# Kernel optimization log

Measured on AMD Instinct MI355X. Metric: run time of the kernel, lower is better.

## Reference

```python
import jax, jax.numpy as jnp
import numpy as np

B = 2048          # batch
F = 32            # input feature size
H = 512           # lstm hidden size
BN = 64           # autoencoder bottleneck
OUT = 8           # final dense output size
SEQ_LEN = 128
LOOK_AHEAD = 32
RS, RE = 0, 8     # replace_start, replace_end (RE-RS == OUT)


def setup_inputs() -> dict:
    key = jax.random.key(0)
    ks = jax.random.split(key, 16)
    s = lambda k, shape: (jax.random.normal(k, shape, jnp.float32) * 0.05)
    return {
        'x': jax.random.normal(ks[0], (B, SEQ_LEN + LOOK_AHEAD, F), jnp.float32),
        # layer-0 LSTMCell (input F)
        'Wih0': s(ks[1], (F, 4 * H)), 'Whh0': s(ks[2], (H, 4 * H)),
        'bih0': s(ks[3], (4 * H,)),   'bhh0': s(ks[4], (4 * H,)),
        # layer-1 LSTMCell (input H)
        'Wih1': s(ks[5], (H, 4 * H)), 'Whh1': s(ks[6], (H, 4 * H)),
        'bih1': s(ks[7], (4 * H,)),   'bhh1': s(ks[8], (4 * H,)),
        # discretizing autoencoder: 2H -> BN -> 2H (shared across layers)
        'We': s(ks[9], (2 * H, BN)),  'be': s(ks[10], (BN,)),
        'Wd': s(ks[11], (BN, 2 * H)), 'bd': s(ks[12], (2 * H,)),
        # final dense H -> OUT
        'Wf': s(ks[13], (H, OUT)),    'bf': s(ks[14], (OUT,)),
    }


def _lstm_cell(x, h, c, Wih, Whh, bih, bhh):
    # torch.nn.LSTMCell gate order: i, f, g, o
    g = x @ Wih + bih + h @ Whh + bhh          # [B, 4H]
    i, f, gg, o = jnp.split(g, 4, axis=1)
    i, f, o = jax.nn.sigmoid(i), jax.nn.sigmoid(f), jax.nn.sigmoid(o)
    c2 = f * c + i * jnp.tanh(gg)
    return o * jnp.tanh(c2), c2


def _ae(z, We, be, Wd, bd):
    # bottleneck with straight-through rounding (discretization)
    b = jnp.tanh(z @ We + be)
    q = b + jax.lax.stop_gradient(jnp.round(b) - b)
    return q @ Wd + bd


def _layers_fwd(x_t, st, p):
    h0, c0, h1, c1 = st
    hc = _ae(jnp.concatenate([h0, c0], axis=1), p['We'], p['be'], p['Wd'], p['bd'])
    h0, c0 = jnp.split(hc, 2, axis=1)
    h0, c0 = _lstm_cell(x_t, h0, c0, p['Wih0'], p['Whh0'], p['bih0'], p['bhh0'])
    # dropout layer between stacked layers is identity in eval mode
    hc = _ae(jnp.concatenate([h1, c1], axis=1), p['We'], p['be'], p['Wd'], p['bd'])
    h1, c1 = jnp.split(hc, 2, axis=1)
    h1, c1 = _lstm_cell(h0, h1, c1, p['Wih1'], p['Whh1'], p['bih1'], p['bhh1'])
    return (h0, c0, h1, c1)


def reference(x, Wih0, Whh0, bih0, bhh0, Wih1, Whh1, bih1, bhh1,
              We, be, Wd, bd, Wf, bf):
    p = dict(Wih0=Wih0, Whh0=Whh0, bih0=bih0, bhh0=bhh0,
             Wih1=Wih1, Whh1=Whh1, bih1=bih1, bhh1=bhh1,
             We=We, be=be, Wd=Wd, bd=bd)
    bsz = x.shape[0]
    z = jnp.zeros((bsz, H), x.dtype)
    st = (z, z, z, z)

    # warm-up phase over seq_len observed steps
    def step1(st, x_t):
        return _layers_fwd(x_t, st, p), None
    st, _ = jax.lax.scan(step1, st, jnp.swapaxes(x[:, :SEQ_LEN], 0, 1))
    out0 = st[2] @ Wf + bf  # final dense on top-layer h

    def step2(carry, x_t):
        st, out = carry
        x_t = x_t.at[:, RS:RE].set(out)
        st = _layers_fwd(x_t, st, p)
        out = st[2] @ Wf + bf
        return (st, out), out
    (_, _), outs = jax.lax.scan(step2, (st, out0),
                                jnp.swapaxes(x[:, SEQ_LEN:SEQ_LEN + LOOK_AHEAD], 0, 1))

    # [B, 1 + look_ahead, OUT]
    return jnp.concatenate([out0[:, None, :], jnp.swapaxes(outs, 0, 1)], axis=1)
```

## Files before the change

### kernel.cpp

```cpp
#include <hip/hip_runtime.h>
#include <hip/hip_bf16.h>
#include <math.h>

#define NB    2048
#define FIN   32
#define HH    512
#define G4    2048
#define BNE   64
#define OUTD  8
#define SEQL  128
#define LOOK  32
#define TOT   (SEQL + LOOK)
#define TB    8
#define NTHR  512

__device__ __forceinline__ float sigf(float v) { return 1.0f / (1.0f + expf(-v)); }

#define MAC8(ACC, W)                                   \
  {                                                    \
    ACC[0] = fmaf(hs0, (W), ACC[0]);                   \
    ACC[1] = fmaf(hs1, (W), ACC[1]);                   \
    ACC[2] = fmaf(hs2, (W), ACC[2]);                   \
    ACC[3] = fmaf(hs3, (W), ACC[3]);                   \
    ACC[4] = fmaf(hs4, (W), ACC[4]);                   \
    ACC[5] = fmaf(hs5, (W), ACC[5]);                   \
    ACC[6] = fmaf(hs6, (W), ACC[6]);                   \
    ACC[7] = fmaf(hs7, (W), ACC[7]);                   \
  }

__global__ __launch_bounds__(NTHR)
void fused_rnn(const float* __restrict__ x,
               const float* __restrict__ Wih0, const float* __restrict__ Whh0,
               const float* __restrict__ bih0, const float* __restrict__ bhh0,
               const float* __restrict__ Wih1, const float* __restrict__ Whh1,
               const float* __restrict__ bih1, const float* __restrict__ bhh1,
               const float* __restrict__ We,   const float* __restrict__ be,
               const float* __restrict__ Wd,   const float* __restrict__ bd,
               const float* __restrict__ Wf,   const float* __restrict__ bf,
               float* __restrict__ out)
{
  __shared__ float sh0[HH][TB], sc0[HH][TB], sh1[HH][TB], sc1[HH][TB];
  __shared__ float sq[2][TB][BNE];
  __shared__ float sx[FIN][TB];
  __shared__ float sout[TB][OUTD];

  const int t  = threadIdx.x;
  const int b0 = blockIdx.x * TB;

  for (int i = t; i < HH * TB; i += NTHR) {
    (&sh0[0][0])[i] = 0.f; (&sc0[0][0])[i] = 0.f;
    (&sh1[0][0])[i] = 0.f; (&sc1[0][0])[i] = 0.f;
  }

  float bias0[4], bias1[4];
#pragma unroll
  for (int j = 0; j < 4; j++) {
    bias0[j] = bih0[j * HH + t] + bhh0[j * HH + t];
    bias1[j] = bih1[j * HH + t] + bhh1[j * HH + t];
  }

  const double Athr = 0.5493061443340549;

  for (int step = 0; step < TOT; ++step) {
    __syncthreads();

    {
      const int ae = t >> 8, s = (t >> 5) & 7, n = t & 31;
      const float* Sh = ae ? &sh1[0][0] : &sh0[0][0];
      const float* Sc = ae ? &sc1[0][0] : &sc0[0][0];
      double a0 = (double)be[n], a1 = (double)be[n + 32];
      const float* we0 = We + n;
#pragma unroll 4
      for (int k = 0; k < HH; k++) {
        double z = (double)Sh[k * TB + s];
        a0 = fma(z, (double)we0[k * BNE], a0);
        a1 = fma(z, (double)we0[k * BNE + 32], a1);
      }
      const float* we1 = We + (size_t)HH * BNE + n;
#pragma unroll 4
      for (int k = 0; k < HH; k++) {
        double z = (double)Sc[k * TB + s];
        a0 = fma(z, (double)we1[k * BNE], a0);
        a1 = fma(z, (double)we1[k * BNE + 32], a1);
      }
      sq[ae][s][n]      = (a0 > Athr) ? 1.f : ((a0 < -Athr) ? -1.f : 0.f);
      sq[ae][s][n + 32] = (a1 > Athr) ? 1.f : ((a1 < -Athr) ? -1.f : 0.f);
    }
    __syncthreads();

    {
      float ah0[TB], ac0[TB], ah1[TB], ac1[TB];
      const float bdh = bd[t], bdc = bd[HH + t];
#pragma unroll
      for (int s = 0; s < TB; s++) { ah0[s] = bdh; ac0[s] = bdc; ah1[s] = bdh; ac1[s] = bdc; }
      const float* wd0 = Wd + t;
      const float* wd1 = Wd + HH + t;
#pragma unroll 2
      for (int j = 0; j < BNE; j++) {
        const float w0 = wd0[j * (2 * HH)];
        const float w1 = wd1[j * (2 * HH)];
#pragma unroll
        for (int s = 0; s < TB; s++) {
          float q0 = sq[0][s][j], q1 = sq[1][s][j];
          ah0[s] = fmaf(q0, w0, ah0[s]); ac0[s] = fmaf(q0, w1, ac0[s]);
          ah1[s] = fmaf(q1, w0, ah1[s]); ac1[s] = fmaf(q1, w1, ac1[s]);
        }
      }
#pragma unroll
      for (int s = 0; s < TB; s++) {
        sh0[t][s] = ah0[s]; sc0[t][s] = ac0[s];
        sh1[t][s] = ah1[s]; sc1[t][s] = ac1[s];
      }
      if (t < FIN * TB) {
        int s = t >> 5, f = t & 31;
        float xv;
        if (step >= SEQL && f < OUTD) xv = sout[s][f];
        else xv = x[((size_t)(b0 + s) * TOT + step) * FIN + f];
        sx[f][s] = xv;
      }
    }
    __syncthreads();

    {
      float accI[TB], accF[TB], accG[TB], accO[TB];
#pragma unroll
      for (int s = 0; s < TB; s++) { accI[s] = bias0[0]; accF[s] = bias0[1]; accG[s] = bias0[2]; accO[s] = bias0[3]; }

      {
        const float* p0 = Wih0 + t;
        const float* p1 = Wih0 + t + 2 * HH;
#pragma unroll 4
        for (int k = 0; k < FIN; k++) {
          float w0 = p0[k * G4], w1 = p0[k * G4 + HH];
          float w2 = p1[k * G4], w3 = p1[k * G4 + HH];
          const float4 hA = *(const float4*)&sx[k][0];
          const float4 hB = *(const float4*)&sx[k][4];
          float hs0 = hA.x, hs1 = hA.y, hs2 = hA.z, hs3 = hA.w;
          float hs4 = hB.x, hs5 = hB.y, hs6 = hB.z, hs7 = hB.w;
          MAC8(accI, w0); MAC8(accF, w1); MAC8(accG, w2); MAC8(accO, w3);
        }
      }
      {
        const float* p0 = Whh0 + t;
        const float* p1 = Whh0 + t + 2 * HH;
#pragma unroll 4
        for (int k = 0; k < HH; k++) {
          float w0 = p0[k * G4], w1 = p0[k * G4 + HH];
          float w2 = p1[k * G4], w3 = p1[k * G4 + HH];
          const float4 hA = *(const float4*)&sh0[k][0];
          const float4 hB = *(const float4*)&sh0[k][4];
          float hs0 = hA.x, hs1 = hA.y, hs2 = hA.z, hs3 = hA.w;
          float hs4 = hB.x, hs5 = hB.y, hs6 = hB.z, hs7 = hB.w;
          MAC8(accI, w0); MAC8(accF, w1); MAC8(accG, w2); MAC8(accO, w3);
        }
      }
      float hn[TB], cn[TB];
      const float4 cA = *(const float4*)&sc0[t][0];
      const float4 cB = *(const float4*)&sc0[t][4];
      float cold[TB] = { cA.x, cA.y, cA.z, cA.w, cB.x, cB.y, cB.z, cB.w };
#pragma unroll
      for (int s = 0; s < TB; s++) {
        float ig = sigf(accI[s]), fg = sigf(accF[s]);
        float gg = tanhf(accG[s]), og = sigf(accO[s]);
        float c2 = fmaf(fg, cold[s], ig * gg);
        cn[s] = c2;
        hn[s] = og * tanhf(c2);
      }
      __syncthreads();
      *(float4*)&sh0[t][0] = make_float4(hn[0], hn[1], hn[2], hn[3]);
      *(float4*)&sh0[t][4] = make_float4(hn[4], hn[5], hn[6], hn[7]);
      *(float4*)&sc0[t][0] = make_float4(cn[0], cn[1], cn[2], cn[3]);
      *(float4*)&sc0[t][4] = make_float4(cn[4], cn[5], cn[6], cn[7]);
    }
    __syncthreads();

    {
      float accI[TB], accF[TB], accG[TB], accO[TB];
#pragma unroll
      for (int s = 0; s < TB; s++) { accI[s] = bias1[0]; accF[s] = bias1[1]; accG[s] = bias1[2]; accO[s] = bias1[3]; }

      {
        const float* p0 = Wih1 + t;
        const float* p1 = Wih1 + t + 2 * HH;
#pragma unroll 4
        for (int k = 0; k < HH; k++) {
          float w0 = p0[k * G4], w1 = p0[k * G4 + HH];
          float w2 = p1[k * G4], w3 = p1[k * G4 + HH];
          const float4 hA = *(const float4*)&sh0[k][0];
          const float4 hB = *(const float4*)&sh0[k][4];
          float hs0 = hA.x, hs1 = hA.y, hs2 = hA.z, hs3 = hA.w;
          float hs4 = hB.x, hs5 = hB.y, hs6 = hB.z, hs7 = hB.w;
          MAC8(accI, w0); MAC8(accF, w1); MAC8(accG, w2); MAC8(accO, w3);
        }
      }
      {
        const float* p0 = Whh1 + t;
        const float* p1 = Whh1 + t + 2 * HH;
#pragma unroll 4
        for (int k = 0; k < HH; k++) {
          float w0 = p0[k * G4], w1 = p0[k * G4 + HH];
          float w2 = p1[k * G4], w3 = p1[k * G4 + HH];
          const float4 hA = *(const float4*)&sh1[k][0];
          const float4 hB = *(const float4*)&sh1[k][4];
          float hs0 = hA.x, hs1 = hA.y, hs2 = hA.z, hs3 = hA.w;
          float hs4 = hB.x, hs5 = hB.y, hs6 = hB.z, hs7 = hB.w;
          MAC8(accI, w0); MAC8(accF, w1); MAC8(accG, w2); MAC8(accO, w3);
        }
      }
      float hn[TB], cn[TB];
      const float4 cA = *(const float4*)&sc1[t][0];
      const float4 cB = *(const float4*)&sc1[t][4];
      float cold[TB] = { cA.x, cA.y, cA.z, cA.w, cB.x, cB.y, cB.z, cB.w };
#pragma unroll
      for (int s = 0; s < TB; s++) {
        float ig = sigf(accI[s]), fg = sigf(accF[s]);
        float gg = tanhf(accG[s]), og = sigf(accO[s]);
        float c2 = fmaf(fg, cold[s], ig * gg);
        cn[s] = c2;
        hn[s] = og * tanhf(c2);
      }
      __syncthreads();
      *(float4*)&sh1[t][0] = make_float4(hn[0], hn[1], hn[2], hn[3]);
      *(float4*)&sh1[t][4] = make_float4(hn[4], hn[5], hn[6], hn[7]);
      *(float4*)&sc1[t][0] = make_float4(cn[0], cn[1], cn[2], cn[3]);
      *(float4*)&sc1[t][4] = make_float4(cn[4], cn[5], cn[6], cn[7]);
    }

    if (step >= SEQL - 1) {
      __syncthreads();
      if (t < TB * OUTD) {
        int s = t >> 3, o = t & 7;
        float a = bf[o];
#pragma unroll 4
        for (int k = 0; k < HH; k++) a = fmaf(sh1[k][s], Wf[k * OUTD + o], a);
        sout[s][o] = a;
        int slot = step - (SEQL - 1);
        out[((size_t)(b0 + s) * (1 + LOOK) + slot) * OUTD + o] = a;
      }
    }
  }
}

extern "C" void kernel_launch(void* const* d_in, const int* in_sizes, int n_in,
                              void* d_out, int out_size, void* d_ws, size_t ws_size,
                              hipStream_t stream) {
  const float* x    = (const float*)d_in[0];
  const float* Wih0 = (const float*)d_in[1];
  const float* Whh0 = (const float*)d_in[2];
  const float* bih0 = (const float*)d_in[3];
  const float* bhh0 = (const float*)d_in[4];
  const float* Wih1 = (const float*)d_in[5];
  const float* Whh1 = (const float*)d_in[6];
  const float* bih1 = (const float*)d_in[7];
  const float* bhh1 = (const float*)d_in[8];
  const float* We   = (const float*)d_in[9];
  const float* be   = (const float*)d_in[10];
  const float* Wd   = (const float*)d_in[11];
  const float* bd   = (const float*)d_in[12];
  const float* Wf   = (const float*)d_in[13];
  const float* bf   = (const float*)d_in[14];

  fused_rnn<<<NB / TB, NTHR, 0, stream>>>(x, Wih0, Whh0, bih0, bhh0,
                                          Wih1, Whh1, bih1, bhh1,
                                          We, be, Wd, bd, Wf, bf,
                                          (float*)d_out);
}
```

Baseline: 89.02 ms.

## Double threads per block and split gate computation via shared gate buffer

Raises the block to 1024 threads. Each thread now computes two adjacent gate columns (float2 weight loads) for all 8 batch rows, writes the pre-activations to a shared gate buffer, and a separate pass applies the LSTM nonlinearities. The encoder and decoder stages are also re-split so each thread handles one bottleneck or output element, and the sq layout is transposed. This exposes more parallelism per recurrent step and gives coalesced float2 weight reads, at the cost of 64KB of extra shared memory, an extra barrier per layer, and fewer registers per thread.

```diff
diff --git a/kernel.cpp b/kernel.cpp
--- a/kernel.cpp
+++ b/kernel.cpp
@@ -12,20 +12,19 @@
 #define LOOK  32
 #define TOT   (SEQL + LOOK)
 #define TB    8
-#define NTHR  512
+#define NTHR  1024
 
 __device__ __forceinline__ float sigf(float v) { return 1.0f / (1.0f + expf(-v)); }
 
-#define MAC8(ACC, W)                                   \
+#define MAC2(S, HS)                                    \
   {                                                    \
-    ACC[0] = fmaf(hs0, (W), ACC[0]);                   \
-    ACC[1] = fmaf(hs1, (W), ACC[1]);                   \
-    ACC[2] = fmaf(hs2, (W), ACC[2]);                   \
-    ACC[3] = fmaf(hs3, (W), ACC[3]);                   \
-    ACC[4] = fmaf(hs4, (W), ACC[4]);                   \
-    ACC[5] = fmaf(hs5, (W), ACC[5]);                   \
-    ACC[6] = fmaf(hs6, (W), ACC[6]);                   \
-    ACC[7] = fmaf(hs7, (W), ACC[7]);                   \
+    a[S].x = fmaf(w.x, (HS), a[S].x);                  \
+    a[S].y = fmaf(w.y, (HS), a[S].y);                  \
+  }
+#define MAC2x8()                                       \
+  {                                                    \
+    MAC2(0, hA.x); MAC2(1, hA.y); MAC2(2, hA.z); MAC2(3, hA.w); \
+    MAC2(4, hB.x); MAC2(5, hB.y); MAC2(6, hB.z); MAC2(7, hB.w); \
   }
 
 __global__ __launch_bounds__(NTHR)
@@ -40,7 +39,8 @@
                float* __restrict__ out)
 {
   __shared__ float sh0[HH][TB], sc0[HH][TB], sh1[HH][TB], sc1[HH][TB];
-  __shared__ float sq[2][TB][BNE];
+  __shared__ float sg[TB][G4];
+  __shared__ float sq[2][BNE][TB];
   __shared__ float sx[FIN][TB];
   __shared__ float sout[TB][OUTD];
 
@@ -52,12 +52,10 @@
     (&sh1[0][0])[i] = 0.f; (&sc1[0][0])[i] = 0.f;
   }
 
-  float bias0[4], bias1[4];
-#pragma unroll
-  for (int j = 0; j < 4; j++) {
-    bias0[j] = bih0[j * HH + t] + bhh0[j * HH + t];
-    bias1[j] = bih1[j * HH + t] + bhh1[j * HH + t];
-  }
+  const float2 bb0 = make_float2(bih0[2*t]   + bhh0[2*t],
+                                 bih0[2*t+1] + bhh0[2*t+1]);
+  const float2 bb1 = make_float2(bih1[2*t]   + bhh1[2*t],
+                                 bih1[2*t+1] + bhh1[2*t+1]);
 
   const double Athr = 0.5493061443340549;
 
@@ -65,51 +63,51 @@
     __syncthreads();
 
     {
-      const int ae = t >> 8, s = (t >> 5) & 7, n = t & 31;
+      const int ae = t >> 9, s = (t >> 6) & 7, n = t & 63;
       const float* Sh = ae ? &sh1[0][0] : &sh0[0][0];
       const float* Sc = ae ? &sc1[0][0] : &sc0[0][0];
-      double a0 = (double)be[n], a1 = (double)be[n + 32];
+      double a0 = (double)be[n];
       const float* we0 = We + n;
 #pragma unroll 4
-      for (int k = 0; k < HH; k++) {
-        double z = (double)Sh[k * TB + s];
-        a0 = fma(z, (double)we0[k * BNE], a0);
-        a1 = fma(z, (double)we0[k * BNE + 32], a1);
-      }
+      for (int k = 0; k < HH; k++)
+        a0 = fma((double)Sh[k * TB + s], (double)we0[(size_t)k * BNE], a0);
       const float* we1 = We + (size_t)HH * BNE + n;
 #pragma unroll 4
-      for (int k = 0; k < HH; k++) {
-        double z = (double)Sc[k * TB + s];
-        a0 = fma(z, (double)we1[k * BNE], a0);
-        a1 = fma(z, (double)we1[k * BNE + 32], a1);
-      }
-      sq[ae][s][n]      = (a0 > Athr) ? 1.f : ((a0 < -Athr) ? -1.f : 0.f);
-      sq[ae][s][n + 32] = (a1 > Athr) ? 1.f : ((a1 < -Athr) ? -1.f : 0.f);
-    }
-    __syncthreads();
-
-    {
-      float ah0[TB], ac0[TB], ah1[TB], ac1[TB];
-      const float bdh = bd[t], bdc = bd[HH + t];
-#pragma unroll
-      for (int s = 0; s < TB; s++) { ah0[s] = bdh; ac0[s] = bdc; ah1[s] = bdh; ac1[s] = bdc; }
-      const float* wd0 = Wd + t;
-      const float* wd1 = Wd + HH + t;
+      for (int k = 0; k < HH; k++)
+        a0 = fma((double)Sc[k * TB + s], (double)we1[(size_t)k * BNE], a0);
+      sq[ae][n][s] = (a0 > Athr) ? 1.f : ((a0 < -Athr) ? -1.f : 0.f);
+    }
+    __syncthreads();
+
+    {
+      float aq0[TB], aq1[TB];
+      const float bdv = bd[t];
+#pragma unroll
+      for (int s = 0; s < TB; s++) { aq0[s] = bdv; aq1[s] = bdv; }
+      const float* wd = Wd + t;
 #pragma unroll 2
       for (int j = 0; j < BNE; j++) {
-        const float w0 = wd0[j * (2 * HH)];
-        const float w1 = wd1[j * (2 * HH)];
-#pragma unroll
-        for (int s = 0; s < TB; s++) {
-          float q0 = sq[0][s][j], q1 = sq[1][s][j];
-          ah0[s] = fmaf(q0, w0, ah0[s]); ac0[s] = fmaf(q0, w1, ac0[s]);
-          ah1[s] = fmaf(q1, w0, ah1[s]); ac1[s] = fmaf(q1, w1, ac1[s]);
-        }
-      }
-#pragma unroll
-      for (int s = 0; s < TB; s++) {
-        sh0[t][s] = ah0[s]; sc0[t][s] = ac0[s];
-        sh1[t][s] = ah1[s]; sc1[t][s] = ac1[s];
+        const float w = wd[(size_t)j * (2 * HH)];
+        const float4 qA0 = *(const float4*)&sq[0][j][0];
+        const float4 qB0 = *(const float4*)&sq[0][j][4];
+        const float4 qA1 = *(const float4*)&sq[1][j][0];
+        const float4 qB1 = *(const float4*)&sq[1][j][4];
+        aq0[0] = fmaf(qA0.x, w, aq0[0]); aq0[1] = fmaf(qA0.y, w, aq0[1]);
+        aq0[2] = fmaf(qA0.z, w, aq0[2]); aq0[3] = fmaf(qA0.w, w, aq0[3]);
+        aq0[4] = fmaf(qB0.x, w, aq0[4]); aq0[5] = fmaf(qB0.y, w, aq0[5]);
+        aq0[6] = fmaf(qB0.z, w, aq0[6]); aq0[7] = fmaf(qB0.w, w, aq0[7]);
+        aq1[0] = fmaf(qA1.x, w, aq1[0]); aq1[1] = fmaf(qA1.y, w, aq1[1]);
+        aq1[2] = fmaf(qA1.z, w, aq1[2]); aq1[3] = fmaf(qA1.w, w, aq1[3]);
+        aq1[4] = fmaf(qB1.x, w, aq1[4]); aq1[5] = fmaf(qB1.y, w, aq1[5]);
+        aq1[6] = fmaf(qB1.z, w, aq1[6]); aq1[7] = fmaf(qB1.w, w, aq1[7]);
+      }
+      if (t < HH) {
+#pragma unroll
+        for (int s = 0; s < TB; s++) { sh0[t][s] = aq0[s]; sh1[t][s] = aq1[s]; }
+      } else {
+        const int c = t - HH;
+#pragma unroll
+        for (int s = 0; s < TB; s++) { sc0[c][s] = aq0[s]; sc1[c][s] = aq1[s]; }
       }
       if (t < FIN * TB) {
         int s = t >> 5, f = t & 31;
@@ -122,108 +120,84 @@
     __syncthreads();
 
     {
-      float accI[TB], accF[TB], accG[TB], accO[TB];
-#pragma unroll
-      for (int s = 0; s < TB; s++) { accI[s] = bias0[0]; accF[s] = bias0[1]; accG[s] = bias0[2]; accO[s] = bias0[3]; }
-
-      {
-        const float* p0 = Wih0 + t;
-        const float* p1 = Wih0 + t + 2 * HH;
-#pragma unroll 4
-        for (int k = 0; k < FIN; k++) {
-          float w0 = p0[k * G4], w1 = p0[k * G4 + HH];
-          float w2 = p1[k * G4], w3 = p1[k * G4 + HH];
-          const float4 hA = *(const float4*)&sx[k][0];
-          const float4 hB = *(const float4*)&sx[k][4];
-          float hs0 = hA.x, hs1 = hA.y, hs2 = hA.z, hs3 = hA.w;
-          float hs4 = hB.x, hs5 = hB.y, hs6 = hB.z, hs7 = hB.w;
-          MAC8(accI, w0); MAC8(accF, w1); MAC8(accG, w2); MAC8(accO, w3);
-        }
-      }
-      {
-        const float* p0 = Whh0 + t;
-        const float* p1 = Whh0 + t + 2 * HH;
-#pragma unroll 4
-        for (int k = 0; k < HH; k++) {
-          float w0 = p0[k * G4], w1 = p0[k * G4 + HH];
-          float w2 = p1[k * G4], w3 = p1[k * G4 + HH];
-          const float4 hA = *(const float4*)&sh0[k][0];
-          const float4 hB = *(const float4*)&sh0[k][4];
-          float hs0 = hA.x, hs1 = hA.y, hs2 = hA.z, hs3 = hA.w;
-          float hs4 = hB.x, hs5 = hB.y, hs6 = hB.z, hs7 = hB.w;
-          MAC8(accI, w0); MAC8(accF, w1); MAC8(accG, w2); MAC8(accO, w3);
-        }
-      }
-      float hn[TB], cn[TB];
-      const float4 cA = *(const float4*)&sc0[t][0];
-      const float4 cB = *(const float4*)&sc0[t][4];
-      float cold[TB] = { cA.x, cA.y, cA.z, cA.w, cB.x, cB.y, cB.z, cB.w };
-#pragma unroll
-      for (int s = 0; s < TB; s++) {
-        float ig = sigf(accI[s]), fg = sigf(accF[s]);
-        float gg = tanhf(accG[s]), og = sigf(accO[s]);
-        float c2 = fmaf(fg, cold[s], ig * gg);
-        cn[s] = c2;
-        hn[s] = og * tanhf(c2);
-      }
-      __syncthreads();
-      *(float4*)&sh0[t][0] = make_float4(hn[0], hn[1], hn[2], hn[3]);
-      *(float4*)&sh0[t][4] = make_float4(hn[4], hn[5], hn[6], hn[7]);
-      *(float4*)&sc0[t][0] = make_float4(cn[0], cn[1], cn[2], cn[3]);
-      *(float4*)&sc0[t][4] = make_float4(cn[4], cn[5], cn[6], cn[7]);
-    }
-    __syncthreads();
-
-    {
-      float accI[TB], accF[TB], accG[TB], accO[TB];
-#pragma unroll
-      for (int s = 0; s < TB; s++) { accI[s] = bias1[0]; accF[s] = bias1[1]; accG[s] = bias1[2]; accO[s] = bias1[3]; }
-
-      {
-        const float* p0 = Wih1 + t;
-        const float* p1 = Wih1 + t + 2 * HH;
-#pragma unroll 4
-        for (int k = 0; k < HH; k++) {
-          float w0 = p0[k * G4], w1 = p0[k * G4 + HH];
-          float w2 = p1[k * G4], w3 = p1[k * G4 + HH];
-          const float4 hA = *(const float4*)&sh0[k][0];
-          const float4 hB = *(const float4*)&sh0[k][4];
-          float hs0 = hA.x, hs1 = hA.y, hs2 = hA.z, hs3 = hA.w;
-          float hs4 = hB.x, hs5 = hB.y, hs6 = hB.z, hs7 = hB.w;
-          MAC8(accI, w0); MAC8(accF, w1); MAC8(accG, w2); MAC8(accO, w3);
-        }
-      }
-      {
-        const float* p0 = Whh1 + t;
-        const float* p1 = Whh1 + t + 2 * HH;
-#pragma unroll 4
-        for (int k = 0; k < HH; k++) {
-          float w0 = p0[k * G4], w1 = p0[k * G4 + HH];
-          float w2 = p1[k * G4], w3 = p1[k * G4 + HH];
-          const float4 hA = *(const float4*)&sh1[k][0];
-          const float4 hB = *(const float4*)&sh1[k][4];
-          float hs0 = hA.x, hs1 = hA.y, hs2 = hA.z, hs3 = hA.w;
-          float hs4 = hB.x, hs5 = hB.y, hs6 = hB.z, hs7 = hB.w;
-          MAC8(accI, w0); MAC8(accF, w1); MAC8(accG, w2); MAC8(accO, w3);
-        }
-      }
-      float hn[TB], cn[TB];
-      const float4 cA = *(const float4*)&sc1[t][0];
-      const float4 cB = *(const float4*)&sc1[t][4];
-      float cold[TB] = { cA.x, cA.y, cA.z, cA.w, cB.x, cB.y, cB.z, cB.w };
-#pragma unroll
-      for (int s = 0; s < TB; s++) {
-        float ig = sigf(accI[s]), fg = sigf(accF[s]);
-        float gg = tanhf(accG[s]), og = sigf(accO[s]);
-        float c2 = fmaf(fg, cold[s], ig * gg);
-        cn[s] = c2;
-        hn[s] = og * tanhf(c2);
-      }
-      __syncthreads();
-      *(float4*)&sh1[t][0] = make_float4(hn[0], hn[1], hn[2], hn[3]);
-      *(float4*)&sh1[t][4] = make_float4(hn[4], hn[5], hn[6], hn[7]);
-      *(float4*)&sc1[t][0] = make_float4(cn[0], cn[1], cn[2], cn[3]);
-      *(float4*)&sc1[t][4] = make_float4(cn[4], cn[5], cn[6], cn[7]);
+      float2 a[TB];
+#pragma unroll
+      for (int s = 0; s < TB; s++) a[s] = bb0;
+      const float2* wx = (const float2*)Wih0 + t;
+#pragma unroll 4
+      for (int k = 0; k < FIN; k++) {
+        const float2 w  = wx[(size_t)k * (G4 / 2)];
+        const float4 hA = *(const float4*)&sx[k][0];
+        const float4 hB = *(const float4*)&sx[k][4];
+        MAC2x8();
+      }
+      const float2* wh = (const float2*)Whh0 + t;
+#pragma unroll 8
+      for (int k = 0; k < HH; k++) {
+        const float2 w  = wh[(size_t)k * (G4 / 2)];
+        const float4 hA = *(const float4*)&sh0[k][0];
+        const float4 hB = *(const float4*)&sh0[k][4];
+        MAC2x8();
+      }
+#pragma unroll
+      for (int s = 0; s < TB; s++) *(float2*)&sg[s][2 * t] = a[s];
+    }
+    __syncthreads();
+    {
+      const int h  = t & (HH - 1);
+      const int sb = (t >> 9) * 4;
+#pragma unroll
+      for (int s2 = 0; s2 < 4; s2++) {
+        const int s = sb + s2;
+        const float ig = sigf(sg[s][h]);
+        const float fg = sigf(sg[s][HH + h]);
+        const float gt = tanhf(sg[s][2 * HH + h]);
+        const float og = sigf(sg[s][3 * HH + h]);
+        const float c2 = fmaf(fg, sc0[h][s], ig * gt);
+        sc0[h][s] = c2;
+        sh0[h][s] = og * tanhf(c2);
+      }
+    }
+    __syncthreads();
+
+    {
+      float2 a[TB];
+#pragma unroll
+      for (int s = 0; s < TB; s++) a[s] = bb1;
+      const float2* wx = (const float2*)Wih1 + t;
+#pragma unroll 8
+      for (int k = 0; k < HH; k++) {
+        const float2 w  = wx[(size_t)k * (G4 / 2)];
+        const float4 hA = *(const float4*)&sh0[k][0];
+        const float4 hB = *(const float4*)&sh0[k][4];
+        MAC2x8();
+      }
+      const float2* wh = (const float2*)Whh1 + t;
+#pragma unroll 8
+      for (int k = 0; k < HH; k++) {
+        const float2 w  = wh[(size_t)k * (G4 / 2)];
+        const float4 hA = *(const float4*)&sh1[k][0];
+        const float4 hB = *(const float4*)&sh1[k][4];
+        MAC2x8();
+      }
+#pragma unroll
+      for (int s = 0; s < TB; s++) *(float2*)&sg[s][2 * t] = a[s];
+    }
+    __syncthreads();
+    {
+      const int h  = t & (HH - 1);
+      const int sb = (t >> 9) * 4;
+#pragma unroll
+      for (int s2 = 0; s2 < 4; s2++) {
+        const int s = sb + s2;
+        const float ig = sigf(sg[s][h]);
+        const float fg = sigf(sg[s][HH + h]);
+        const float gt = tanhf(sg[s][2 * HH + h]);
+        const float og = sigf(sg[s][3 * HH + h]);
+        const float c2 = fmaf(fg, sc1[h][s], ig * gt);
+        sc1[h][s] = c2;
+        sh1[h][s] = og * tanhf(c2);
+      }
     }
 
     if (step >= SEQL - 1) {
```

New measurement: 81.12 ms. -8.9%, faster.
